# Kernel optimization log

Hardware: AMD Instinct MI355X
Metric: run time of the kernel (lower is better)

The kernel has to match this reference:

```python
import jax, jax.numpy as jnp
import numpy as np

N = 20000   # nodes per graph
E = 320000  # edges per graph
D_IN, D_H = 128, 304


def _param(key, shape, fan_in):
    return jax.random.normal(key, shape, dtype=jnp.float32) / np.sqrt(fan_in)


def setup_inputs() -> dict:
    key = jax.random.key(0)
    ks = jax.random.split(key, 20)
    inp = {}
    for i, name in enumerate(['x1', 'x2', 'x3']):
        inp[name] = jax.random.normal(ks[i], (N, D_IN), dtype=jnp.float32)
    for i, name in enumerate(['src1', 'dst1', 'src2', 'dst2', 'src3', 'dst3']):
        inp[name] = jax.random.randint(ks[3 + i], (E,), 0, N, dtype=jnp.int32)
    # shared GraphConv weights (DGL GraphConv: h = norm_agg(x) @ W + b)
    inp['W1'] = _param(ks[9], (D_IN, D_H), D_IN)
    inp['b1'] = jnp.zeros((D_H,), jnp.float32)
    inp['W2'] = _param(ks[10], (D_H, D_H), D_H)
    inp['b2'] = jnp.zeros((D_H,), jnp.float32)
    inp['W3'] = _param(ks[11], (D_H, D_H), D_H)
    inp['b3'] = jnp.zeros((D_H,), jnp.float32)
    # MLP head: 304 -> 128 -> 64 -> 1
    inp['fW1'] = _param(ks[12], (D_H, 128), D_H)
    inp['fb1'] = jnp.zeros((128,), jnp.float32)
    inp['fW2'] = _param(ks[13], (128, 64), 128)
    inp['fb2'] = jnp.zeros((64,), jnp.float32)
    inp['fW3'] = _param(ks[14], (64, 1), 64)
    inp['fb3'] = jnp.zeros((1,), jnp.float32)
    return inp


def gcn_conv(x, src, dst, W, b):
    # DGL GraphConv, norm='both': h = D_in^{-1/2} A D_out^{-1/2} x W + b
    ones = jnp.ones((src.shape[0],), x.dtype)
    out_deg = jnp.clip(jax.ops.segment_sum(ones, src, num_segments=N), 1.0)
    in_deg = jnp.clip(jax.ops.segment_sum(ones, dst, num_segments=N), 1.0)
    h = x * jax.lax.rsqrt(out_deg)[:, None]
    agg = jax.ops.segment_sum(h[src], dst, num_segments=N)  # [N, d] SpMM
    agg = agg * jax.lax.rsqrt(in_deg)[:, None]
    return agg @ W + b


def reference(x1, x2, x3, src1, dst1, src2, dst2, src3, dst3,
              W1, b1, W2, b2, W3, b3, fW1, fb1, fW2, fb2, fW3, fb3):
    def branch(x, src, dst):
        x = jax.nn.relu(gcn_conv(x, src, dst, W1, b1))
        x = jax.nn.relu(gcn_conv(x, src, dst, W2, b2))
        x = jax.nn.relu(gcn_conv(x, src, dst, W3, b3))
        return x

    h1 = branch(x1, src1, dst1)
    h2 = branch(x2, src2, dst2)
    h3 = branch(x3, src3, dst3)
    # multi_graph_opt='max': max over all nodes of all three graphs -> [304]
    pooled = jnp.max(jnp.concatenate([h1, h2, h3], axis=0), axis=0)
    # output_opt='fc': MLP head with sigmoid
    z = jax.nn.relu(pooled @ fW1 + fb1)
    z = jax.nn.relu(z @ fW2 + fb2)
    return jax.nn.sigmoid(z @ fW3 + fb3)  # shape [1]
```

## Files before the change

kernel.cpp:

```cpp
#include <hip/hip_runtime.h>
#include <hip/hip_bf16.h>
#include <math.h>

#define NODES 20000
#define EDGES 320000
#define NB 3
#define TOTN (NODES * NB)
#define TOTE (EDGES * NB)
#define D_IN 128
#define D_H 304
#define SCAN_B 59
#define SLICES 40
#define SLICE_E (EDGES / SLICES)
#define ZX TOTN
#define ZQ (TOTN + 96)
#define PACKB 7500
#define PREPWB 960

typedef __attribute__((ext_vector_type(4))) float f32x4;
typedef __attribute__((ext_vector_type(2))) float f32x2;

__device__ __forceinline__ void gload16(const void* g, void* l) {
    __builtin_amdgcn_global_load_lds(
        (const __attribute__((address_space(1))) unsigned*)g,
        (__attribute__((address_space(3))) unsigned*)l, 16, 0, 0);
}

__global__ __launch_bounds__(1024, 1) void k_hist(
    const int* __restrict__ s1, const int* __restrict__ d1,
    const int* __restrict__ s2, const int* __restrict__ d2,
    const int* __restrict__ s3, const int* __restrict__ d3,
    unsigned short* __restrict__ partial_in, unsigned short* __restrict__ partial_out,
    int* __restrict__ gctr) {
    __shared__ unsigned hist[NODES / 2];
    if (blockIdx.x == 0 && blockIdx.y == 0 && threadIdx.x == 0) *gctr = 0;
    int g = blockIdx.x / SLICES, s = blockIdx.x % SLICES;
    bool isOut = (blockIdx.y == 1);
    const int* ep;
    if (isOut) ep = (g == 0) ? s1 : ((g == 1) ? s2 : s3);
    else       ep = (g == 0) ? d1 : ((g == 1) ? d2 : d3);
    ep += s * SLICE_E;
    for (int i = threadIdx.x; i < NODES / 2; i += 1024) hist[i] = 0;
    __syncthreads();
    const int4* ep4 = (const int4*)ep;
    for (int i = threadIdx.x; i < SLICE_E / 4; i += 1024) {
        int4 v = ep4[i];
        atomicAdd(&hist[v.x >> 1], 1u << ((v.x & 1) << 4));
        atomicAdd(&hist[v.y >> 1], 1u << ((v.y & 1) << 4));
        atomicAdd(&hist[v.z >> 1], 1u << ((v.z & 1) << 4));
        atomicAdd(&hist[v.w >> 1], 1u << ((v.w & 1) << 4));
    }
    __syncthreads();
    unsigned* po = (unsigned*)((isOut ? partial_out : partial_in) + (size_t)blockIdx.x * NODES);
    for (int i = threadIdx.x; i < NODES / 2; i += 1024) po[i] = hist[i];
}

__global__ void k_degscan(const unsigned short* __restrict__ partial_in,
                          const unsigned short* __restrict__ partial_out,
                          float* __restrict__ inv_in, float* __restrict__ inv_out,
                          int* __restrict__ row_ptr, int* __restrict__ rend,
                          int* __restrict__ O, int* __restrict__ gctr) {
    __shared__ int wsum[16];
    __shared__ int sbase;
    int b = blockIdx.x, t = threadIdx.x;
    int i = b * 1024 + t;
    int lane = t & 63, wid = t >> 6;
    int v = 0;
    int g = 0, ln = 0;
    if (i < TOTN) {
        g = i / NODES; ln = i - g * NODES;
        const unsigned short* pi = partial_in + (size_t)g * SLICES * NODES + ln;
        const unsigned short* po = partial_out + (size_t)g * SLICES * NODES + ln;
        int ci = 0, co = 0;
        #pragma unroll
        for (int s = 0; s < SLICES; s++) { ci += pi[s * NODES]; co += po[s * NODES]; }
        v = ci;
        inv_in[i]  = 1.0f / sqrtf((float)max(ci, 1));
        inv_out[i] = 1.0f / sqrtf((float)max(co, 1));
    }
    int sv = v;
    #pragma unroll
    for (int o = 1; o < 64; o <<= 1) {
        int u = __shfl_up(sv, o, 64);
        if (lane >= o) sv += u;
    }
    if (lane == 63) wsum[wid] = sv;
    __syncthreads();
    if (t < 16) {
        int w = wsum[t];
        #pragma unroll
        for (int o = 1; o < 16; o <<= 1) {
            int u = __shfl_up(w, o, 16);
            if (t >= o) w += u;
        }
        wsum[t] = w;
    }
    __syncthreads();
    if (t == 0) sbase = atomicAdd(gctr, wsum[15]);
    __syncthreads();
    int wbase = (wid > 0) ? wsum[wid - 1] : 0;
    if (i < TOTN) {
        int rp = sbase + wbase + sv - v;
        row_ptr[i] = rp;
        rend[i] = rp + v;
        const unsigned short* pi = partial_in + (size_t)g * SLICES * NODES + ln;
        int* on = O + (size_t)g * SLICES * NODES + ln;
        int run = rp;
        #pragma unroll
        for (int s = 0; s < SLICES; s++) {
            on[s * NODES] = run;
            run += pi[s * NODES];
        }
    }
}

__global__ void k_prep(const float4* __restrict__ x1, const float4* __restrict__ x2,
                       const float4* __restrict__ x3, const float* __restrict__ inv_out,
                       unsigned* __restrict__ q,
                       const float* __restrict__ W1, const float* __restrict__ W2,
                       const float* __restrict__ W3,
                       unsigned char* __restrict__ Wt1, unsigned char* __restrict__ Wt2,
                       unsigned char* __restrict__ Wt3,
                       int* __restrict__ csr_slack, unsigned* __restrict__ x8z,
                       unsigned* __restrict__ q8z, int* __restrict__ pooled) {
    if (blockIdx.x < PACKB) {
        const int per = NODES * D_IN / 4;
        int i = blockIdx.x * 256 + threadIdx.x;
        const float4* s; int j;
        if (i < per)          { s = x1; j = i; }
        else if (i < 2 * per) { s = x2; j = i - per; }
        else                  { s = x3; j = i - 2 * per; }
        float4 v = s[j];
        float sc = inv_out[i >> 5];
        int p = __builtin_amdgcn_cvt_pk_fp8_f32(v.x * sc, v.y * sc, 0, false);
        p = __builtin_amdgcn_cvt_pk_fp8_f32(v.z * sc, v.w * sc, p, true);
        q[i] = (unsigned)p;
    } else if (blockIdx.x < PACKB + PREPWB) {
        const int N1 = 320 * 128, N2 = 320 * 320;
        int id = (blockIdx.x - PACKB) * 256 + threadIdx.x;
        const float* W; unsigned char* Wt; int K, Kpad, lid;
        if (id < N1)                { W = W1; Wt = Wt1; K = 128; Kpad = 128; lid = id; }
        else if (id < N1 + N2)      { W = W2; Wt = Wt2; K = 304; Kpad = 320; lid = id - N1; }
        else                        { W = W3; Wt = Wt3; K = 304; Kpad = 320; lid = id - N1 - N2; }
        int n = lid / Kpad, k = lid - n * Kpad;
        unsigned char v = 0;
        if (k < K && n < D_H) {
            float w = W[k * D_H + n];
            v = (unsigned char)(__builtin_amdgcn_cvt_pk_fp8_f32(w, w, 0, false) & 0xff);
        }
        Wt[lid] = v;
    } else {
        int ex = threadIdx.x;
        if (ex < 32) csr_slack[ex] = 0;
        else if (ex < 64) x8z[ex - 32] = 0;
        else if (ex < 144) q8z[ex - 64] = 0;
        else if (ex < 464) pooled[ex - 144] = 0;
    }
}

__global__ __launch_bounds__(1024, 1) void k_fill2(
    const int* __restrict__ s1, const int* __restrict__ d1,
    const int* __restrict__ s2, const int* __restrict__ d2,
    const int* __restrict__ s3, const int* __restrict__ d3,
    const int* __restrict__ O, int* __restrict__ csr) {
    __shared__ int cur[NODES];
    int g = blockIdx.x / SLICES, s = blockIdx.x % SLICES;
    const int* sp = (g == 0) ? s1 : ((g == 1) ? s2 : s3);
    const int* dp = (g == 0) ? d1 : ((g == 1) ? d2 : d3);
    sp += s * SLICE_E; dp += s * SLICE_E;
    const int* on = O + (size_t)blockIdx.x * NODES;
    for (int i = threadIdx.x; i < NODES; i += 1024) cur[i] = on[i];
    __syncthreads();
    int base = g * NODES;
    const int4* sp4 = (const int4*)sp;
    const int4* dp4 = (const int4*)dp;
    for (int i = threadIdx.x; i < SLICE_E / 4; i += 1024) {
        int4 dv = dp4[i];
        int4 sv = sp4[i];
        int p0 = atomicAdd(&cur[dv.x], 1); csr[p0] = sv.x + base;
        int p1 = atomicAdd(&cur[dv.y], 1); csr[p1] = sv.y + base;
        int p2 = atomicAdd(&cur[dv.z], 1); csr[p2] = sv.z + base;
        int p3 = atomicAdd(&cur[dv.w], 1); csr[p3] = sv.w + base;
    }
}

__global__ void k_spmm_l1(const uint2* __restrict__ h, unsigned char* __restrict__ agg,
                          const int* __restrict__ row_ptr, const int* __restrict__ rend,
                          const int* __restrict__ csr,
                          const float* __restrict__ inv_in) {
    int n = blockIdx.x * 4 + (threadIdx.x >> 6);
    int lane = threadIdx.x & 63;
    int s = lane >> 4;
    int off = lane & 15;
    f32x2 a[4];
    #pragma unroll
    for (int j = 0; j < 4; j++) a[j] = (f32x2){0.f, 0.f};
    int k0 = row_ptr[n], k1 = rend[n];
    int deg = k1 - k0;
    const int* cp = csr + k0 + s;
    int e[8];
    #pragma unroll
    for (int j = 0; j < 8; j++) {
        int ev = cp[4 * j];
        e[j] = (s + 4 * j < deg) ? ev : ZX;
    }
    uint2 u[8];
    #pragma unroll
    for (int j = 0; j < 8; j++)
        if (4 * j < deg) u[j] = h[(size_t)e[j] * 16 + off];
    #pragma unroll
    for (int j = 0; j < 8; j++) {
        if (4 * j < deg) {
            a[0] += __builtin_amdgcn_cvt_pk_f32_fp8(u[j].x, false);
            a[1] += __builtin_amdgcn_cvt_pk_f32_fp8(u[j].x, true);
            a[2] += __builtin_amdgcn_cvt_pk_f32_fp8(u[j].y, false);
            a[3] += __builtin_amdgcn_cvt_pk_f32_fp8(u[j].y, true);
        }
    }
    for (int k = k0 + 32 + s; k < k1; k += 4) {
        int e0 = csr[k];
        uint2 u0 = h[(size_t)e0 * 16 + off];
        a[0] += __builtin_amdgcn_cvt_pk_f32_fp8(u0.x, false);
        a[1] += __builtin_amdgcn_cvt_pk_f32_fp8(u0.x, true);
        a[2] += __builtin_amdgcn_cvt_pk_f32_fp8(u0.y, false);
        a[3] += __builtin_amdgcn_cvt_pk_f32_fp8(u0.y, true);
    }
    float r[8];
    #pragma unroll
    for (int j = 0; j < 4; j++) {
        #pragma unroll
        for (int c = 0; c < 2; c++) {
            float v = a[j][c];
            r[2 * j + c] = v + __shfl(v, lane + 16, 64)
                             + __shfl(v, lane + 32, 64)
                             + __shfl(v, lane + 48, 64);
        }
    }
    if (lane < 16) {
        float wi = inv_in[n];
        int d0 = __builtin_amdgcn_cvt_pk_fp8_f32(r[0] * wi, r[1] * wi, 0, false);
        d0 = __builtin_amdgcn_cvt_pk_fp8_f32(r[2] * wi, r[3] * wi, d0, true);
        int d1 = __builtin_amdgcn_cvt_pk_fp8_f32(r[4] * wi, r[5] * wi, 0, false);
        d1 = __builtin_amdgcn_cvt_pk_fp8_f32(r[6] * wi, r[7] * wi, d1, true);
        uint2 st; st.x = (unsigned)d0; st.y = (unsigned)d1;
        *(uint2*)(agg + (size_t)n * 128 + lane * 8) = st;
    }
}

__global__ void k_spmm_big(const uint4* __restrict__ h, unsigned char* __restrict__ agg,
                           const int* __restrict__ row_ptr, const int* __restrict__ rend,
                           const int* __restrict__ csr,
                           const float* __restrict__ inv_in) {
    int n = blockIdx.x * 4 + (threadIdx.x >> 6);
    int lane = threadIdx.x & 63;
    int s = lane / 20;
    int off = lane % 20;
    f32x2 a[8];
    #pragma unroll
    for (int j = 0; j < 8; j++) a[j] = (f32x2){0.f, 0.f};
    int k0 = row_ptr[n], k1 = rend[n];
    int deg = k1 - k0;
    int degg = (s < 3) ? deg : 0;
    const int* cp = csr + k0 + s;
    int e[8];
    #pragma unroll
    for (int j = 0; j < 8; j++) {
        int ev = cp[3 * j];
        e[j] = (s + 3 * j < degg) ? ev : ZQ;
    }
    uint4 u[8];
    #pragma unroll
    for (int j = 0; j < 8; j++)
        if (3 * j < deg) u[j] = h[(size_t)e[j] * 20 + off];
    #pragma unroll
    for (int j = 0; j < 8; j++) {
        if (3 * j < deg) {
            a[0] += __builtin_amdgcn_cvt_pk_f32_fp8(u[j].x, false);
            a[1] += __builtin_amdgcn_cvt_pk_f32_fp8(u[j].x, true);
            a[2] += __builtin_amdgcn_cvt_pk_f32_fp8(u[j].y, false);
            a[3] += __builtin_amdgcn_cvt_pk_f32_fp8(u[j].y, true);
            a[4] += __builtin_amdgcn_cvt_pk_f32_fp8(u[j].z, false);
            a[5] += __builtin_amdgcn_cvt_pk_f32_fp8(u[j].z, true);
            a[6] += __builtin_amdgcn_cvt_pk_f32_fp8(u[j].w, false);
            a[7] += __builtin_amdgcn_cvt_pk_f32_fp8(u[j].w, true);
        }
    }
    int k1g = k0 + degg;
    for (int k = k0 + 24 + s; k < k1g; k += 3) {
        int e0 = csr[k];
        uint4 u0 = h[(size_t)e0 * 20 + off];
        a[0] += __builtin_amdgcn_cvt_pk_f32_fp8(u0.x, false);
        a[1] += __builtin_amdgcn_cvt_pk_f32_fp8(u0.x, true);
        a[2] += __builtin_amdgcn_cvt_pk_f32_fp8(u0.y, false);
        a[3] += __builtin_amdgcn_cvt_pk_f32_fp8(u0.y, true);
        a[4] += __builtin_amdgcn_cvt_pk_f32_fp8(u0.z, false);
        a[5] += __builtin_amdgcn_cvt_pk_f32_fp8(u0.z, true);
        a[6] += __builtin_amdgcn_cvt_pk_f32_fp8(u0.w, false);
        a[7] += __builtin_amdgcn_cvt_pk_f32_fp8(u0.w, true);
    }
    float r[16];
    #pragma unroll
    for (int j = 0; j < 8; j++) {
        #pragma unroll
        for (int c = 0; c < 2; c++) {
            float v = a[j][c];
            r[2 * j + c] = v + __shfl(v, lane + 20, 64) + __shfl(v, lane + 40, 64);
        }
    }
    if (lane < 20) {
        float wi = inv_in[n];
        int d0 = __builtin_amdgcn_cvt_pk_fp8_f32(r[0] * wi, r[1] * wi, 0, false);
        d0 = __builtin_amdgcn_cvt_pk_fp8_f32(r[2] * wi, r[3] * wi, d0, true);
        int d1 = __builtin_amdgcn_cvt_pk_fp8_f32(r[4] * wi, r[5] * wi, 0, false);
        d1 = __builtin_amdgcn_cvt_pk_fp8_f32(r[6] * wi, r[7] * wi, d1, true);
        int d2 = __builtin_amdgcn_cvt_pk_fp8_f32(r[8] * wi, r[9] * wi, 0, false);
        d2 = __builtin_amdgcn_cvt_pk_fp8_f32(r[10] * wi, r[11] * wi, d2, true);
        int d3 = __builtin_amdgcn_cvt_pk_fp8_f32(r[12] * wi, r[13] * wi, 0, false);
        d3 = __builtin_amdgcn_cvt_pk_fp8_f32(r[14] * wi, r[15] * wi, d3, true);
        uint4 st; st.x = (unsigned)d0; st.y = (unsigned)d1; st.z = (unsigned)d2; st.w = (unsigned)d3;
        *(uint4*)(agg + (size_t)n * 320 + lane * 16) = st;
    }
}

template <int MODE>
__global__ __launch_bounds__(256, 2) void k_gemm_mfma(
    const unsigned char* __restrict__ A, int lda,
    const unsigned char* __restrict__ Wt,
    const float* __restrict__ bias,
    const float* __restrict__ inv_out,
    unsigned char* __restrict__ C8, int* __restrict__ gpool, int M, int K) {
    __shared__ char SM[57344];
    __shared__ int pmax[D_H];
    int tid = threadIdx.x;
    int wv = tid >> 6, lane = tid & 63;
    int quad = lane >> 4, lrow = lane & 15;
    int bm = blockIdx.x * 128;

    if (MODE == 1) {
        for (int i = tid; i < D_H; i += 256) pmax[i] = 0;
    }

    f32x4 acc[2][19];
    #pragma unroll
    for (int r = 0; r < 2; r++)
        #pragma unroll
        for (int t = 0; t < 19; t++) acc[r][t] = (f32x4){0.f, 0.f, 0.f, 0.f};

    int swz = (lrow & 3) ^ (lrow >> 2);
    int hb = (quad & 1) * 8;

    auto stage = [&](int buf, int kt) {
        char* As = SM + buf * 28672;
        char* Bs = As + 8192;
        #pragma unroll
        for (int j = 0; j < 2; j++) {
            int c = j * 256 + tid;
            int row = c >> 2, xc = c & 3;
            int col = xc ^ (row & 3) ^ ((row >> 2) & 3);
            gload16(A + (size_t)(bm + row) * lda + kt + col * 16, As + c * 16);
        }
        #pragma unroll
        for (int j = 0; j < 5; j++) {
            int c = j * 256 + tid;
            int row = c >> 2, xc = c & 3;
            int col = xc ^ (row & 3) ^ ((row >> 2) & 3);
            gload16(Wt + (size_t)row * K + kt + col * 16, Bs + c * 16);
        }
    };

    int nt = K >> 6;
    stage(0, 0);
    __syncthreads();
    for (int t = 0; t < nt; t++) {
        if (t + 1 < nt) stage((t + 1) & 1, (t + 1) << 6);
        const char* As = SM + (t & 1) * 28672;
        const char* Bs = As + 8192;
        #pragma unroll
        for (int sub = 0; sub < 2; sub++) {
            int c0 = sub * 2 + (quad >> 1);
            int cx = (c0 ^ swz) * 16 + hb;
            int ra = wv * 32 + lrow;
            long long a0 = *(const long long*)(As + ra * 64 + cx);
            long long a1 = *(const long long*)(As + (ra + 16) * 64 + cx);
            #pragma unroll
            for (int u = 0; u < 19; u++) {
                long long b = *(const long long*)(Bs + (u * 16 + lrow) * 64 + cx);
                acc[0][u] = __builtin_amdgcn_mfma_f32_16x16x32_fp8_fp8(a0, b, acc[0][u], 0, 0, 0);
                acc[1][u] = __builtin_amdgcn_mfma_f32_16x16x32_fp8_fp8(a1, b, acc[1][u], 0, 0, 0);
            }
        }
        __syncthreads();
    }
    if (MODE == 0) {
        unsigned char* OUT = (unsigned char*)SM;
        if (tid < 128) *(uint4*)(OUT + tid * 320 + 304) = make_uint4(0u, 0u, 0u, 0u);
        #pragma unroll
        for (int t = 0; t < 19; t++) {
            int col = t * 16 + lrow;
            float bv = bias[col];
            #pragma unroll
            for (int r = 0; r < 2; r++) {
                int rl = wv * 32 + r * 16 + quad * 4;
                #pragma unroll
                for (int g = 0; g < 4; g++) {
                    int row = bm + rl + g;
                    float sc = inv_out[min(row, M - 1)];
                    float v = fmaxf(acc[r][t][g] + bv, 0.f) * sc;
                    int p = __builtin_amdgcn_cvt_pk_fp8_f32(v, v, 0, false);
                    OUT[(rl + g) * 320 + col] = (unsigned char)(p & 0xff);
                }
            }
        }
        __syncthreads();
        #pragma unroll
        for (int j = 0; j < 10; j++) {
            int c = j * 256 + tid;
            *(uint4*)(C8 + (size_t)bm * 320 + (size_t)c * 16) = *(const uint4*)(OUT + c * 16);
        }
    } else {
        #pragma unroll
        for (int t = 0; t < 19; t++) {
            int col = t * 16 + lrow;
            float bv = bias[col];
            float m = 0.f;
            #pragma unroll
            for (int r = 0; r < 2; r++) {
                int rbase = bm + wv * 32 + r * 16 + quad * 4;
                #pragma unroll
                for (int g = 0; g < 4; g++) {
                    int row = rbase + g;
                    if (row < M) m = fmaxf(m, fmaxf(acc[r][t][g] + bv, 0.f));
                }
            }
            atomicMax(&pmax[col], __float_as_int(m));
        }
        __syncthreads();
        for (int i = tid; i < D_H; i += 256)
            atomicMax(&gpool[i], pmax[i]);
    }
}

__global__ void k_mlp(const int* __restrict__ pooled_i,
                      const float* __restrict__ fW1, const float* __restrict__ fb1,
                      const float* __restrict__ fW2, const float* __restrict__ fb2,
                      const float* __restrict__ fW3, const float* __restrict__ fb3,
                      float* __restrict__ out) {
    __shared__ float p[D_H];
    __shared__ float z1[128];
    __shared__ float z2[64];
    int t = threadIdx.x;
    if (t < D_H) p[t] = __int_as_float(pooled_i[t]);
    __syncthreads();
    if (t < 128) {
        float acc = fb1[t];
        for (int k = 0; k < D_H; k++) acc += p[k] * fW1[k * 128 + t];
        z1[t] = fmaxf(acc, 0.f);
    }
    __syncthreads();
    if (t < 64) {
        float acc = fb2[t];
        for (int k = 0; k < 128; k++) acc += z1[k] * fW2[k * 64 + t];
        z2[t] = fmaxf(acc, 0.f);
    }
    __syncthreads();
    if (t == 0) {
        float acc = fb3[0];
        for (int k = 0; k < 64; k++) acc += z2[k] * fW3[k];
        out[0] = 1.f / (1.f + expf(-acc));
    }
}

extern "C" void kernel_launch(void* const* d_in, const int* in_sizes, int n_in,
                              void* d_out, int out_size, void* d_ws, size_t ws_size,
                              hipStream_t stream) {
    const float* x1 = (const float*)d_in[0];
    const float* x2 = (const float*)d_in[1];
    const float* x3 = (const float*)d_in[2];
    const int* src1 = (const int*)d_in[3];
    const int* dst1 = (const int*)d_in[4];
    const int* src2 = (const int*)d_in[5];
    const int* dst2 = (const int*)d_in[6];
    const int* src3 = (const int*)d_in[7];
    const int* dst3 = (const int*)d_in[8];
    const float* W1 = (const float*)d_in[9];
    const float* b1 = (const float*)d_in[10];
    const float* W2 = (const float*)d_in[11];
    const float* b2 = (const float*)d_in[12];
    const float* W3 = (const float*)d_in[13];
    const float* b3 = (const float*)d_in[14];
    const float* fW1 = (const float*)d_in[15];
    const float* fb1 = (const float*)d_in[16];
    const float* fW2 = (const float*)d_in[17];
    const float* fb2 = (const float*)d_in[18];
    const float* fW3 = (const float*)d_in[19];
    const float* fb3 = (const float*)d_in[20];
    float* out = (float*)d_out;

    char* w = (char*)d_ws;
    unsigned* X8       = (unsigned*)w;      w += (size_t)(TOTN + 1) * 32 * 4;
    unsigned char* Q8  = (unsigned char*)w; w += (size_t)(TOTN + 128) * 320;
    unsigned char* P8  = (unsigned char*)w; w += (size_t)(TOTN + 128) * 320;
    unsigned char* Wt1 = (unsigned char*)w; w += (size_t)320 * 128;
    unsigned char* Wt2 = (unsigned char*)w; w += (size_t)320 * 320;
    unsigned char* Wt3 = (unsigned char*)w; w += (size_t)320 * 320;
    w = (char*)(((size_t)w + 255) & ~(size_t)255);
    unsigned short* partial_in  = (unsigned short*)w; w += (size_t)NB * SLICES * NODES * 2;
    unsigned short* partial_out = (unsigned short*)w; w += (size_t)NB * SLICES * NODES * 2;
    int* O         = (int*)w;    w += (size_t)NB * SLICES * NODES * 4;
    float* inv_out = (float*)w;  w += (size_t)TOTN * 4;
    float* inv_in  = (float*)w;  w += (size_t)TOTN * 4;
    int* row_ptr   = (int*)w;    w += (size_t)TOTN * 4;
    int* rend      = (int*)w;    w += (size_t)TOTN * 4;
    int* csr       = (int*)w;    w += (size_t)(TOTE + 32) * 4;
    int* pooled    = (int*)w;    w += 320 * 4;
    int* gctr      = (int*)w;    w += 64;

    k_hist<<<dim3(NB * SLICES, 2), 1024, 0, stream>>>(src1, dst1, src2, dst2, src3, dst3,
                                                      partial_in, partial_out, gctr);
    k_degscan<<<SCAN_B, 1024, 0, stream>>>(partial_in, partial_out,
                                           inv_in, inv_out, row_ptr, rend, O, gctr);
    k_prep<<<PACKB + PREPWB + 1, 256, 0, stream>>>(
        (const float4*)x1, (const float4*)x2, (const float4*)x3, inv_out, X8,
        W1, W2, W3, Wt1, Wt2, Wt3,
        csr + TOTE, X8 + (size_t)ZX * 32, (unsigned*)(Q8 + (size_t)ZQ * 320), pooled);
    k_fill2<<<NB * SLICES, 1024, 0, stream>>>(src1, dst1, src2, dst2, src3, dst3, O, csr);

    int ggrid = (TOTN + 127) / 128;

    k_spmm_l1<<<TOTN / 4, 256, 0, stream>>>((const uint2*)X8, P8, row_ptr, rend, csr, inv_in);
    k_gemm_mfma<0><<<ggrid, 256, 0, stream>>>(P8, 128, Wt1, b1, inv_out,
                                              Q8, nullptr, TOTN, 128);
    k_spmm_big<<<TOTN / 4, 256, 0, stream>>>((const uint4*)Q8, P8, row_ptr, rend, csr, inv_in);
    k_gemm_mfma<0><<<ggrid, 256, 0, stream>>>(P8, 320, Wt2, b2, inv_out,
                                              Q8, nullptr, TOTN, 320);
    k_spmm_big<<<TOTN / 4, 256, 0, stream>>>((const uint4*)Q8, P8, row_ptr, rend, csr, inv_in);
    k_gemm_mfma<1><<<ggrid, 256, 0, stream>>>(P8, 320, Wt3, b3, nullptr,
                                              nullptr, pooled, TOTN, 320);

    k_mlp<<<1, 320, 0, stream>>>(pooled, fW1, fb1, fW2, fb2, fW3, fb3, out);
}
```

Baseline: 317.0 us.

## Keep full weight matrix resident in LDS and merge CSR fill with prep kernel

The MFMA GEMM now loads the entire padded fp8 weight matrix into shared memory once per block and streams only A tiles with double buffering. It also doubles the block to 512 threads covering 256 rows and templates on K. Separately, the CSR fill kernel is merged into the input-packing/weight-prep kernel, which removes one launch and lets those blocks overlap. The GEMM change cuts repeated B reloads per k-step, at the cost of a larger LDS footprint (up to about 130KB), which may reduce occupancy. The zero padding after the Q8/P8 buffers is enlarged to cover the bigger row tiles.

```diff
diff --git a/kernel.cpp b/kernel.cpp
--- a/kernel.cpp
+++ b/kernel.cpp
@@ -13,9 +13,10 @@
 #define SLICES 40
 #define SLICE_E (EDGES / SLICES)
 #define ZX TOTN
-#define ZQ (TOTN + 96)
-#define PACKB 7500
-#define PREPWB 960
+#define ZQ (TOTN + 192)
+#define FILLB 120
+#define PACK1B 1875
+#define PREPW1B 240
 
 typedef __attribute__((ext_vector_type(4))) float f32x4;
 typedef __attribute__((ext_vector_type(2))) float f32x2;
@@ -114,18 +115,44 @@
     }
 }
 
-__global__ void k_prep(const float4* __restrict__ x1, const float4* __restrict__ x2,
-                       const float4* __restrict__ x3, const float* __restrict__ inv_out,
-                       unsigned* __restrict__ q,
-                       const float* __restrict__ W1, const float* __restrict__ W2,
-                       const float* __restrict__ W3,
-                       unsigned char* __restrict__ Wt1, unsigned char* __restrict__ Wt2,
-                       unsigned char* __restrict__ Wt3,
-                       int* __restrict__ csr_slack, unsigned* __restrict__ x8z,
-                       unsigned* __restrict__ q8z, int* __restrict__ pooled) {
-    if (blockIdx.x < PACKB) {
+__global__ __launch_bounds__(1024, 1) void k_fillprep(
+    const int* __restrict__ s1, const int* __restrict__ d1,
+    const int* __restrict__ s2, const int* __restrict__ d2,
+    const int* __restrict__ s3, const int* __restrict__ d3,
+    const int* __restrict__ O, int* __restrict__ csr,
+    const float4* __restrict__ x1, const float4* __restrict__ x2,
+    const float4* __restrict__ x3, const float* __restrict__ inv_out,
+    unsigned* __restrict__ q,
+    const float* __restrict__ W1, const float* __restrict__ W2,
+    const float* __restrict__ W3,
+    unsigned char* __restrict__ Wt1, unsigned char* __restrict__ Wt2,
+    unsigned char* __restrict__ Wt3,
+    int* __restrict__ csr_slack, unsigned* __restrict__ x8z,
+    unsigned* __restrict__ q8z, int* __restrict__ pooled) {
+    __shared__ int cur[NODES];
+    int b = blockIdx.x;
+    if (b < FILLB) {
+        int g = b / SLICES, s = b % SLICES;
+        const int* sp = (g == 0) ? s1 : ((g == 1) ? s2 : s3);
+        const int* dp = (g == 0) ? d1 : ((g == 1) ? d2 : d3);
+        sp += s * SLICE_E; dp += s * SLICE_E;
+        const int* on = O + (size_t)b * NODES;
+        for (int i = threadIdx.x; i < NODES; i += 1024) cur[i] = on[i];
+        __syncthreads();
+        int base = g * NODES;
+        const int4* sp4 = (const int4*)sp;
+        const int4* dp4 = (const int4*)dp;
+        for (int i = threadIdx.x; i < SLICE_E / 4; i += 1024) {
+            int4 dv = dp4[i];
+            int4 sv = sp4[i];
+            int p0 = atomicAdd(&cur[dv.x], 1); csr[p0] = sv.x + base;
+            int p1 = atomicAdd(&cur[dv.y], 1); csr[p1] = sv.y + base;
+            int p2 = atomicAdd(&cur[dv.z], 1); csr[p2] = sv.z + base;
+            int p3 = atomicAdd(&cur[dv.w], 1); csr[p3] = sv.w + base;
+        }
+    } else if (b < FILLB + PACK1B) {
         const int per = NODES * D_IN / 4;
-        int i = blockIdx.x * 256 + threadIdx.x;
+        int i = (b - FILLB) * 1024 + threadIdx.x;
         const float4* s; int j;
         if (i < per)          { s = x1; j = i; }
         else if (i < 2 * per) { s = x2; j = i - per; }
@@ -135,9 +162,9 @@
         int p = __builtin_amdgcn_cvt_pk_fp8_f32(v.x * sc, v.y * sc, 0, false);
         p = __builtin_amdgcn_cvt_pk_fp8_f32(v.z * sc, v.w * sc, p, true);
         q[i] = (unsigned)p;
-    } else if (blockIdx.x < PACKB + PREPWB) {
+    } else if (b < FILLB + PACK1B + PREPW1B) {
         const int N1 = 320 * 128, N2 = 320 * 320;
-        int id = (blockIdx.x - PACKB) * 256 + threadIdx.x;
+        int id = (b - FILLB - PACK1B) * 1024 + threadIdx.x;
         const float* W; unsigned char* Wt; int K, Kpad, lid;
         if (id < N1)                { W = W1; Wt = Wt1; K = 128; Kpad = 128; lid = id; }
         else if (id < N1 + N2)      { W = W2; Wt = Wt2; K = 304; Kpad = 320; lid = id - N1; }
@@ -155,32 +182,6 @@
         else if (ex < 64) x8z[ex - 32] = 0;
         else if (ex < 144) q8z[ex - 64] = 0;
         else if (ex < 464) pooled[ex - 144] = 0;
-    }
-}
-
-__global__ __launch_bounds__(1024, 1) void k_fill2(
-    const int* __restrict__ s1, const int* __restrict__ d1,
-    const int* __restrict__ s2, const int* __restrict__ d2,
-    const int* __restrict__ s3, const int* __restrict__ d3,
-    const int* __restrict__ O, int* __restrict__ csr) {
-    __shared__ int cur[NODES];
-    int g = blockIdx.x / SLICES, s = blockIdx.x % SLICES;
-    const int* sp = (g == 0) ? s1 : ((g == 1) ? s2 : s3);
-    const int* dp = (g == 0) ? d1 : ((g == 1) ? d2 : d3);
-    sp += s * SLICE_E; dp += s * SLICE_E;
-    const int* on = O + (size_t)blockIdx.x * NODES;
-    for (int i = threadIdx.x; i < NODES; i += 1024) cur[i] = on[i];
-    __syncthreads();
-    int base = g * NODES;
-    const int4* sp4 = (const int4*)sp;
-    const int4* dp4 = (const int4*)dp;
-    for (int i = threadIdx.x; i < SLICE_E / 4; i += 1024) {
-        int4 dv = dp4[i];
-        int4 sv = sp4[i];
-        int p0 = atomicAdd(&cur[dv.x], 1); csr[p0] = sv.x + base;
-        int p1 = atomicAdd(&cur[dv.y], 1); csr[p1] = sv.y + base;
-        int p2 = atomicAdd(&cur[dv.z], 1); csr[p2] = sv.z + base;
-        int p3 = atomicAdd(&cur[dv.w], 1); csr[p3] = sv.w + base;
     }
 }
 
@@ -322,23 +323,22 @@
     }
 }
 
-template <int MODE>
-__global__ __launch_bounds__(256, 2) void k_gemm_mfma(
-    const unsigned char* __restrict__ A, int lda,
+template <int MODE, int K>
+__global__ __launch_bounds__(512, 2) void k_gemm_mfma(
+    const unsigned char* __restrict__ A,
     const unsigned char* __restrict__ Wt,
     const float* __restrict__ bias,
     const float* __restrict__ inv_out,
-    unsigned char* __restrict__ C8, int* __restrict__ gpool, int M, int K) {
-    __shared__ char SM[57344];
-    __shared__ int pmax[D_H];
+    unsigned char* __restrict__ C8, int* __restrict__ gpool, int M) {
+    constexpr int BSZ = 320 * K;
+    constexpr int SMSZ = (BSZ + 32768 > 81920) ? BSZ + 32768 : 81920;
+    __shared__ char SM[SMSZ];
+    char* Bs = SM;
+    char* As0 = SM + BSZ;
     int tid = threadIdx.x;
     int wv = tid >> 6, lane = tid & 63;
     int quad = lane >> 4, lrow = lane & 15;
-    int bm = blockIdx.x * 128;
-
-    if (MODE == 1) {
-        for (int i = tid; i < D_H; i += 256) pmax[i] = 0;
-    }
+    int bm = blockIdx.x * 256;
 
     f32x4 acc[2][19];
     #pragma unroll
@@ -349,42 +349,52 @@
     int swz = (lrow & 3) ^ (lrow >> 2);
     int hb = (quad & 1) * 8;
 
-    auto stage = [&](int buf, int kt) {
-        char* As = SM + buf * 28672;
-        char* Bs = As + 8192;
-        #pragma unroll
-        for (int j = 0; j < 2; j++) {
-            int c = j * 256 + tid;
-            int row = c >> 2, xc = c & 3;
+    constexpr int CPR = K / 16;
+    constexpr int NBC = 320 * CPR;
+    #pragma unroll
+    for (int j = 0; j < (NBC + 511) / 512; j++) {
+        int c = j * 512 + tid;
+        if (c < NBC) {
+            int row = c / CPR, ws = c - row * CPR;
+            int seg = ws >> 2, xc = ws & 3;
             int col = xc ^ (row & 3) ^ ((row >> 2) & 3);
-            gload16(A + (size_t)(bm + row) * lda + kt + col * 16, As + c * 16);
-        }
-        #pragma unroll
-        for (int j = 0; j < 5; j++) {
-            int c = j * 256 + tid;
-            int row = c >> 2, xc = c & 3;
-            int col = xc ^ (row & 3) ^ ((row >> 2) & 3);
-            gload16(Wt + (size_t)row * K + kt + col * 16, Bs + c * 16);
-        }
-    };
-
-    int nt = K >> 6;
-    stage(0, 0);
-    __syncthreads();
-    for (int t = 0; t < nt; t++) {
-        if (t + 1 < nt) stage((t + 1) & 1, (t + 1) << 6);
-        const char* As = SM + (t & 1) * 28672;
-        const char* Bs = As + 8192;
+            gload16(Wt + (size_t)row * K + seg * 64 + col * 16, Bs + c * 16);
+        }
+    }
+    #pragma unroll
+    for (int j = 0; j < 2; j++) {
+        int c = j * 512 + tid;
+        int row = c >> 2, xc = c & 3;
+        int col = xc ^ (row & 3) ^ ((row >> 2) & 3);
+        gload16(A + (size_t)(bm + row) * K + col * 16, As0 + c * 16);
+    }
+    __syncthreads();
+
+    constexpr int NT = K / 64;
+    for (int t = 0; t < NT; t++) {
+        const char* Asc = As0 + (t & 1) * 16384;
+        if (t + 1 < NT) {
+            char* Asn = As0 + ((t + 1) & 1) * 16384;
+            int ktn = (t + 1) << 6;
+            #pragma unroll
+            for (int j = 0; j < 2; j++) {
+                int c = j * 512 + tid;
+                int row = c >> 2, xc = c & 3;
+                int col = xc ^ (row & 3) ^ ((row >> 2) & 3);
+                gload16(A + (size_t)(bm + row) * K + ktn + col * 16, Asn + c * 16);
+            }
+        }
+        int kt = t << 6;
         #pragma unroll
         for (int sub = 0; sub < 2; sub++) {
             int c0 = sub * 2 + (quad >> 1);
             int cx = (c0 ^ swz) * 16 + hb;
             int ra = wv * 32 + lrow;
-            long long a0 = *(const long long*)(As + ra * 64 + cx);
-            long long a1 = *(const long long*)(As + (ra + 16) * 64 + cx);
+            long long a0 = *(const long long*)(Asc + ra * 64 + cx);
+            long long a1 = *(const long long*)(Asc + (ra + 16) * 64 + cx);
             #pragma unroll
             for (int u = 0; u < 19; u++) {
-                long long b = *(const long long*)(Bs + (u * 16 + lrow) * 64 + cx);
+                long long b = *(const long long*)(Bs + (size_t)(u * 16 + lrow) * K + kt + cx);
                 acc[0][u] = __builtin_amdgcn_mfma_f32_16x16x32_fp8_fp8(a0, b, acc[0][u], 0, 0, 0);
                 acc[1][u] = __builtin_amdgcn_mfma_f32_16x16x32_fp8_fp8(a1, b, acc[1][u], 0, 0, 0);
             }
@@ -393,7 +403,7 @@
     }
     if (MODE == 0) {
         unsigned char* OUT = (unsigned char*)SM;
-        if (tid < 128) *(uint4*)(OUT + tid * 320 + 304) = make_uint4(0u, 0u, 0u, 0u);
+        if (tid < 256) *(uint4*)(OUT + tid * 320 + 304) = make_uint4(0u, 0u, 0u, 0u);
         #pragma unroll
         for (int t = 0; t < 19; t++) {
             int col = t * 16 + lrow;
@@ -414,10 +424,13 @@
         __syncthreads();
         #pragma unroll
         for (int j = 0; j < 10; j++) {
-            int c = j * 256 + tid;
+            int c = j * 512 + tid;
             *(uint4*)(C8 + (size_t)bm * 320 + (size_t)c * 16) = *(const uint4*)(OUT + c * 16);
         }
     } else {
+        int* pmax = (int*)SM;
+        for (int i = tid; i < D_H; i += 512) pmax[i] = 0;
+        __syncthreads();
         #pragma unroll
         for (int t = 0; t < 19; t++) {
             int col = t * 16 + lrow;
@@ -435,7 +448,7 @@
             atomicMax(&pmax[col], __float_as_int(m));
         }
         __syncthreads();
-        for (int i = tid; i < D_H; i += 256)
+        for (int i = tid; i < D_H; i += 512)
             atomicMax(&gpool[i], pmax[i]);
     }
 }
@@ -498,8 +511,8 @@
 
     char* w = (char*)d_ws;
     unsigned* X8       = (unsigned*)w;      w += (size_t)(TOTN + 1) * 32 * 4;
-    unsigned char* Q8  = (unsigned char*)w; w += (size_t)(TOTN + 128) * 320;
-    unsigned char* P8  = (unsigned char*)w; w += (size_t)(TOTN + 128) * 320;
+    unsigned char* Q8  = (unsigned char*)w; w += (size_t)(TOTN + 320) * 320;
+    unsigned char* P8  = (unsigned char*)w; w += (size_t)(TOTN + 320) * 320;
     unsigned char* Wt1 = (unsigned char*)w; w += (size_t)320 * 128;
     unsigned char* Wt2 = (unsigned char*)w; w += (size_t)320 * 320;
     unsigned char* Wt3 = (unsigned char*)w; w += (size_t)320 * 320;
@@ -519,23 +532,23 @@
                                                       partial_in, partial_out, gctr);
     k_degscan<<<SCAN_B, 1024, 0, stream>>>(partial_in, partial_out,
                                            inv_in, inv_out, row_ptr, rend, O, gctr);
-    k_prep<<<PACKB + PREPWB + 1, 256, 0, stream>>>(
+    k_fillprep<<<FILLB + PACK1B + PREPW1B + 1, 1024, 0, stream>>>(
+        src1, dst1, src2, dst2, src3, dst3, O, csr,
         (const float4*)x1, (const float4*)x2, (const float4*)x3, inv_out, X8,
         W1, W2, W3, Wt1, Wt2, Wt3,
         csr + TOTE, X8 + (size_t)ZX * 32, (unsigned*)(Q8 + (size_t)ZQ * 320), pooled);
-    k_fill2<<<NB * SLICES, 1024, 0, stream>>>(src1, dst1, src2, dst2, src3, dst3, O, csr);
-
-    int ggrid = (TOTN + 127) / 128;
+
+    int ggrid = (TOTN + 255) / 256;
 
     k_spmm_l1<<<TOTN / 4, 256, 0, stream>>>((const uint2*)X8, P8, row_ptr, rend, csr, inv_in);
-    k_gemm_mfma<0><<<ggrid, 256, 0, stream>>>(P8, 128, Wt1, b1, inv_out,
-                                              Q8, nullptr, TOTN, 128);
+    k_gemm_mfma<0, 128><<<ggrid, 512, 0, stream>>>(P8, Wt1, b1, inv_out,
+                                                   Q8, nullptr, TOTN);
     k_spmm_big<<<TOTN / 4, 256, 0, stream>>>((const uint4*)Q8, P8, row_ptr, rend, csr, inv_in);
-    k_gemm_mfma<0><<<ggrid, 256, 0, stream>>>(P8, 320, Wt2, b2, inv_out,
-                                              Q8, nullptr, TOTN, 320);
+    k_gemm_mfma<0, 320><<<ggrid, 512, 0, stream>>>(P8, Wt2, b2, inv_out,
+                                                   Q8, nullptr, TOTN);
     k_spmm_big<<<TOTN / 4, 256, 0, stream>>>((const uint4*)Q8, P8, row_ptr, rend, csr, inv_in);
-    k_gemm_mfma<1><<<ggrid, 256, 0, stream>>>(P8, 320, Wt3, b3, nullptr,
-                                              nullptr, pooled, TOTN, 320);
+    k_gemm_mfma<1, 320><<<ggrid, 512, 0, stream>>>(P8, Wt3, b3, nullptr,
+                                                   nullptr, pooled, TOTN);
 
     k_mlp<<<1, 320, 0, stream>>>(pooled, fW1, fb1, fW2, fb2, fW3, fb3, out);
 }
```

Measured after the change: 316.3 us. No clear change (-0.2%).
